# Kernel optimization log

Measured on AMD Instinct MI355X. Metric: run time of the kernel, lower is better.

Reference implementation:

```python
import jax, jax.numpy as jnp
import numpy as np

K, T, CIN = 30000, 35, 7
EPS = 1e-5  # torch BatchNorm default


def _bn(x, gamma, beta):
    # x: [1, K, T, C]; per-channel batch-stat normalization over (0,1,2)
    mean = jnp.mean(x, axis=(0, 1, 2))
    var = jnp.var(x, axis=(0, 1, 2))
    return (x - mean) * jax.lax.rsqrt(var + EPS) * gamma + beta


def _vfe(x, mask, W, b, gamma, beta):
    # x: [1, K, T, Cin] -> [1, K, T, 2*units]
    pw = jnp.einsum('bkti,iu->bktu', x, W) + b
    pw = jax.nn.relu(_bn(pw, gamma, beta))
    agg = jnp.max(pw, axis=2, keepdims=True)            # [1, K, 1, units]
    out = jnp.concatenate([pw, jnp.broadcast_to(agg, pw.shape)], axis=-1)
    return out * mask


def setup_inputs() -> dict:
    key = jax.random.key(0)
    ks = jax.random.split(key, 8)
    inp = {}
    inp['x'] = jax.random.normal(ks[0], (K, T, CIN), jnp.float32)
    inp['coordinate'] = jax.random.randint(ks[1], (K, 4), 0, 1, dtype=jnp.int32)
    inp['batch_size'] = 1
    inp['W1'] = jax.random.normal(ks[2], (7, 16), jnp.float32) * 0.3
    inp['b1'] = jnp.zeros((16,), jnp.float32)
    inp['g1'] = jnp.ones((16,), jnp.float32)
    inp['be1'] = jnp.zeros((16,), jnp.float32)
    inp['W2'] = jax.random.normal(ks[3], (32, 64), jnp.float32) * 0.15
    inp['b2'] = jnp.zeros((64,), jnp.float32)
    inp['g2'] = jnp.ones((64,), jnp.float32)
    inp['be2'] = jnp.zeros((64,), jnp.float32)
    inp['Wd'] = jax.random.normal(ks[4], (128, 128), jnp.float32) * 0.1
    inp['bd'] = jnp.zeros((128,), jnp.float32)
    inp['gd'] = jnp.ones((128,), jnp.float32)
    inp['bed'] = jnp.zeros((128,), jnp.float32)
    return inp


def reference(x, coordinate, batch_size, W1, b1, g1, be1, W2, b2, g2, be2, Wd, bd, gd, bed):
    xb = x[None]                                   # [1, K, T, 7]
    # mask: 1 where the point's feature sum is nonzero
    mask = (jnp.sum(xb, axis=-1) != 0.0).astype(jnp.float32)[..., None]  # [1,K,T,1]
    h = _vfe(xb, mask, W1, b1, g1, be1)            # [1, K, T, 32]
    h = _vfe(h, mask, W2, b2, g2, be2)             # [1, K, T, 128]
    h = jnp.einsum('bktc,cd->bktd', h, Wd) + bd    # [1, K, T, 128]
    h = _bn(h, gd, bed)                            # BatchNorm2d after permute(0,3,1,2)
    h = jnp.where(h >= 0, h, 0.1 * h)              # leaky_relu(0.1)
    h = jnp.max(h, axis=2)                         # max over points -> [1, K, 128]
    out = jnp.transpose(h, (0, 2, 1))              # [1, 128, K] to match NCHW layout
    return (out, coordinate)
```

## Files before the change

### kernel.cpp

```cpp
#include <hip/hip_runtime.h>

#define KVOX 30000
#define TP 35
#define NPTS (KVOX * TP)
#define EPS_BN 1e-5f

typedef __attribute__((ext_vector_type(8))) short short8_t;
typedef __attribute__((ext_vector_type(4))) float f32x4;

#define MFMA_BF16 __builtin_amdgcn_mfma_f32_16x16x32_bf16

#define SLOTG_OFF 0
#define SLOT2_OFF 2560
#define SLOT3_OFF 10752
#define PAR_A1 27136
#define PAR_C1 27152
#define PAR_A2 27168
#define PAR_C2 27232
#define PAR_A3 27296
#define PAR_C3 27424
#define STATS_FLOATS 27136
#define W2T_OFF 27552
#define WDT_OFF 28576
#define M3_OFF 36768
#define SMALL_FLOATS (36768 + KVOX * 64)
#define H1G_OFF SMALL_FLOATS
#define REC_DW 1224
#define FULL_FLOATS (H1G_OFF + (KVOX / 4) * REC_DW)

__device__ __forceinline__ ushort f2bf(float f) {
    uint r;
    asm("v_cvt_pk_bf16_f32 %0, %1, %2" : "=v"(r) : "v"(f), "v"(f));
    return (ushort)r;
}
__device__ __forceinline__ uint f2bf2(float lo, float hi) {
    uint r;
    asm("v_cvt_pk_bf16_f32 %0, %1, %2" : "=v"(r) : "v"(lo), "v"(hi));
    return r;
}
__device__ __forceinline__ float bf2f(ushort h) {
    union { uint u; float f; } v; v.u = ((uint)h) << 16; return v.f;
}
__device__ __forceinline__ f32x4 vmax4(f32x4 a, f32x4 b) {
    f32x4 r;
    r[0] = fmaxf(a[0], b[0]); r[1] = fmaxf(a[1], b[1]);
    r[2] = fmaxf(a[2], b[2]); r[3] = fmaxf(a[3], b[3]);
    return r;
}

__global__ __launch_bounds__(256) void k_prep_stats1(
    const float* __restrict__ x,
    const float* __restrict__ W2, const float* __restrict__ Wd,
    const float* __restrict__ gd,
    ushort* __restrict__ w2t, ushort* __restrict__ wdt,
    float* __restrict__ slotG) {
    if (blockIdx.x < 64) {
        int t = blockIdx.x * 256 + threadIdx.x;
        if (t < 2048) {
            int u = t >> 5, k = t & 31;
            w2t[t] = f2bf(W2[k * 64 + u]);
        }
        int u = t >> 7, k = t & 127;
        float sg = (gd[u] < 0.f) ? -1.f : 1.f;
        wdt[t] = f2bf(Wd[k * 128 + u] * sg);
        return;
    }
    int bid = blockIdx.x - 64;
    int tid = threadIdx.x;
    int gid = bid * 256 + tid;
    float sx[7], G[28];
#pragma unroll
    for (int c = 0; c < 7; ++c) sx[c] = 0.f;
#pragma unroll
    for (int i = 0; i < 28; ++i) G[i] = 0.f;
    for (size_t p4 = (size_t)gid * 4; p4 < NPTS; p4 += (size_t)131072 * 4) {
        const f32x4* xp = (const f32x4*)(x + p4 * 7);
        f32x4 q[7];
#pragma unroll
        for (int c = 0; c < 7; ++c) q[c] = xp[c];
#pragma unroll
        for (int j = 0; j < 4; ++j) {
            float xv[7];
#pragma unroll
            for (int c = 0; c < 7; ++c) {
                int idx = j * 7 + c;
                xv[c] = q[idx >> 2][idx & 3];
                sx[c] += xv[c];
            }
            int idx = 0;
#pragma unroll
            for (int i = 0; i < 7; ++i)
#pragma unroll
                for (int jj = i; jj < 7; ++jj) { G[idx] = fmaf(xv[i], xv[jj], G[idx]); ++idx; }
        }
    }
    int lane = tid & 63;
    int wv = tid >> 6;
    int slot = (bid * 4 + wv) & 63;
#pragma unroll
    for (int k = 0; k < 35; ++k) {
        float v = (k < 28) ? G[k] : sx[k - 28];
#pragma unroll
        for (int m = 32; m > 0; m >>= 1) v += __shfl_xor(v, m, 64);
        if (lane == 0) atomicAdd(&slotG[slot * 40 + k], v);
    }
}

__global__ void k_affine1g(const float* __restrict__ slotG,
                           const float* __restrict__ W1, const float* __restrict__ b1,
                           const float* __restrict__ g1, const float* __restrict__ be1,
                           float* __restrict__ pa, float* __restrict__ pc, float invN) {
    __shared__ float red[35];
    int t = threadIdx.x;
    if (t < 35) {
        float s = 0.f;
#pragma unroll
        for (int sl = 0; sl < 64; ++sl) s += slotG[sl * 40 + t];
        red[t] = s;
    }
    __syncthreads();
    if (t < 16) {
        float wv[7];
#pragma unroll
        for (int c = 0; c < 7; ++c) wv[c] = W1[c * 16 + t];
        float b = b1[t];
        float sw = 0.f;
#pragma unroll
        for (int c = 0; c < 7; ++c) sw = fmaf(red[28 + c], wv[c], sw);
        float gq = 0.f;
        int idx = 0;
#pragma unroll
        for (int i = 0; i < 7; ++i)
#pragma unroll
            for (int j = i; j < 7; ++j) {
                float coef = wv[i] * wv[j];
                if (i != j) coef *= 2.f;
                gq = fmaf(coef, red[idx], gq);
                ++idx;
            }
        float mr = sw * invN;
        float mean = mr + b;
        float ex2 = gq * invN + 2.f * b * mr + b * b;
        float var = ex2 - mean * mean;
        float av = g1[t] * rsqrtf(var + EPS_BN);
        pa[t] = av;
        pc[t] = be1[t] - mean * av;
    }
}

__global__ void k_affine_b(const float* __restrict__ slots,
                           const float* __restrict__ g,
                           const float* __restrict__ be,
                           const float* __restrict__ bias,
                           float* __restrict__ pa, float* __restrict__ pc,
                           int C, float invN) {
    int u = threadIdx.x;
    if (u >= C) return;
    float s = 0.f, q = 0.f;
    for (int sl = 0; sl < 64; ++sl) {
        s += slots[sl * 2 * C + u];
        q += slots[sl * 2 * C + C + u];
    }
    float b = bias[u];
    float mr = s * invN;
    float mean = mr + b;
    float ex2 = q * invN + 2.f * b * mr + b * b;
    float var = ex2 - mean * mean;
    float av = g[u] * rsqrtf(var + EPS_BN);
    pa[u] = av;
    pc[u] = be[u] - mean * av;
}

__global__ void k_affine_b3(const float* __restrict__ slots,
                            const float* __restrict__ g,
                            const float* __restrict__ be,
                            const float* __restrict__ bias,
                            float* __restrict__ pa, float* __restrict__ pc,
                            int C, float invN) {
    int u = threadIdx.x;
    if (u >= C) return;
    float s = 0.f, q = 0.f;
    for (int sl = 0; sl < 64; ++sl) {
        s += slots[sl * 2 * C + u];
        q += slots[sl * 2 * C + C + u];
    }
    float sg = (g[u] < 0.f) ? -1.f : 1.f;
    s *= sg;
    float b = bias[u];
    float mr = s * invN;
    float mean = mr + b;
    float ex2 = q * invN + 2.f * b * mr + b * b;
    float var = ex2 - mean * mean;
    float av = g[u] * rsqrtf(var + EPS_BN);
    pa[u] = av;
    pc[u] = be[u] - mean * av;
}

__device__ __forceinline__ void phaseA4(
    int k0, int tid,
    const float* __restrict__ x,
    const float* __restrict__ W1, const float* __restrict__ b1,
    const float* __restrict__ a1, const float* __restrict__ c1,
    ushort* __restrict__ h1, float* __restrict__ lmask,
    float* __restrict__ aggp , ushort* __restrict__ agg1bf ) {
    int u = tid & 15;
    int g = tid >> 4;
    int v = g & 3;
    int th = g >> 2;
    float pmax = 0.f;
    if (th < 7) {
        float b1u = b1[u];
        float a1u = a1[u], c1u = c1[u];
        float w1c[7];
#pragma unroll
        for (int c = 0; c < 7; ++c) w1c[c] = W1[c * 16 + u];
#pragma unroll
        for (int i = 0; i < 5; ++i) {
            int t = th * 5 + i;
            const float* xp = x + ((size_t)(k0 + v) * TP + t) * 7;
            float xv[7];
            float sum7 = 0.f;
#pragma unroll
            for (int c = 0; c < 7; ++c) { xv[c] = xp[c]; sum7 += xv[c]; }
            float mkv = (sum7 != 0.f) ? 1.f : 0.f;
            int row = 4 * t + v;
            if (u == 0) lmask[row] = mkv;
            float val = b1u;
#pragma unroll
            for (int c = 0; c < 7; ++c) val = fmaf(xv[c], w1c[c], val);
            val = fmaxf(fmaf(a1u, val, c1u), 0.f);
            pmax = fmaxf(pmax, val);
            h1[row * 24 + u] = f2bf(val * mkv);
        }
    } else {
        int row = 140 + v;
        h1[row * 24 + u] = 0;
        if (u == 0) lmask[row] = 0.f;
    }
    int w = tid >> 6;
    int lane = tid & 63;
    if (w < 7) aggp[w * 64 + lane] = pmax;
    __syncthreads();
    if (tid < 64) {
        float m = aggp[tid];
#pragma unroll
        for (int ww = 1; ww < 7; ++ww) m = fmaxf(m, aggp[ww * 64 + tid]);
        agg1bf[tid] = f2bf(m);
    }
    __syncthreads();
}

template <bool DUMP>
__global__ __launch_bounds__(512, 8) void k_stats2(
    const float* __restrict__ x,
    const float* __restrict__ W1, const float* __restrict__ b1,
    const ushort* __restrict__ w2t,
    const float* __restrict__ ws,
    float* __restrict__ slot2, uint* __restrict__ recs) {
    __shared__ __align__(16) ushort h1[144 * 24];
    __shared__ float lmask[144];
    __shared__ float aggp[7 * 64];
    __shared__ __align__(16) ushort agg1bf[64];
    __shared__ __align__(16) uint zeros16[4];
    int tid = threadIdx.x;
    int k0 = blockIdx.x * 4;
    if (tid < 4) zeros16[tid] = 0;
    phaseA4(k0, tid, x, W1, b1, ws + PAR_A1, ws + PAR_C1, h1, lmask, aggp, agg1bf);
    if (DUMP) {
        uint* rec = recs + (size_t)blockIdx.x * REC_DW;
        const uint* h1dw = (const uint*)h1;
        for (int i = tid; i < 1120; i += 512) rec[i] = h1dw[(i >> 3) * 12 + (i & 7)];
        if (tid < 32) rec[1120 + tid] = ((const uint*)agg1bf)[tid];
        if (tid < 70) rec[1152 + tid] = f2bf2(lmask[2 * tid], lmask[2 * tid + 1]);
    }
    int w = tid >> 6, lane = tid & 63, lq = lane >> 4, lr = lane & 15;
    int mh = w >> 2, uq = w & 3;
    int u = uq * 16 + lr;
    short8_t bB = *(const short8_t*)(w2t + u * 32 + (lq & 1) * 8);
    short8_t bP = *(const short8_t*)(w2t + u * 32 + 16 + (lq & 1) * 8);
    const ushort* pap = (lq < 2) ? (agg1bf + (lr & 3) * 16 + (lq & 1) * 8) : (const ushort*)zeros16;
    short8_t pAf = *(const short8_t*)pap;
    f32x4 aP = {0.f, 0.f, 0.f, 0.f};
    aP = MFMA_BF16(pAf, bP, aP, 0, 0, 0);
    f32x4 p1;
    p1[0] = __shfl(aP[0], lr, 64); p1[1] = __shfl(aP[1], lr, 64);
    p1[2] = __shfl(aP[2], lr, 64); p1[3] = __shfl(aP[3], lr, 64);
    f32x4 s1p = {0.f, 0.f, 0.f, 0.f}, s2p = {0.f, 0.f, 0.f, 0.f};
    int mt0 = mh ? 5 : 0, mt1 = mh ? 9 : 5;
    for (int mt = mt0; mt < mt1; ++mt) {
        const ushort* ha = (lq < 2) ? (h1 + (mt * 16 + lr) * 24 + (lq & 1) * 8) : (const ushort*)zeros16;
        short8_t af = *(const short8_t*)ha;
        f32x4 acc = {0.f, 0.f, 0.f, 0.f};
        acc = MFMA_BF16(af, bB, acc, 0, 0, 0);
        f32x4 mk = *(const f32x4*)(lmask + mt * 16 + lq * 4);
        f32x4 am = (acc + p1) * mk;
        s1p += am;
        s2p += am * am;
    }
    float s1 = s1p[0] + s1p[1] + s1p[2] + s1p[3];
    float s2 = s2p[0] + s2p[1] + s2p[2] + s2p[3];
    s1 += __shfl_xor(s1, 16, 64); s1 += __shfl_xor(s1, 32, 64);
    s2 += __shfl_xor(s2, 16, 64); s2 += __shfl_xor(s2, 32, 64);
    if (lq == 0) {
        int slot = blockIdx.x & 63;
        atomicAdd(&slot2[slot * 128 + u], s1);
        atomicAdd(&slot2[slot * 128 + 64 + u], s2);
    }
}

__global__ __launch_bounds__(512, 8) void k_stage3_reuse(
    const uint* __restrict__ recs,
    const float* __restrict__ b2,
    const ushort* __restrict__ w2t, const ushort* __restrict__ wdt,
    const float* __restrict__ bd, const float* __restrict__ gd,
    const float* __restrict__ ws,
    float* __restrict__ slot3, ushort* __restrict__ m3) {
    __shared__ __align__(16) ushort h1[144 * 24];
    __shared__ __align__(16) ushort h2[144 * 72];
    __shared__ float lmask[144];
    __shared__ __align__(16) uint aggfU[4 * 68];
    __shared__ __align__(16) ushort agg1bf[64];
    __shared__ __align__(16) uint zeros16[4];
    int tid = threadIdx.x;
    int k0 = blockIdx.x * 4;
    int w = tid >> 6, lane = tid & 63, lq = lane >> 4, lr = lane & 15;

    {
        const uint* rec = recs + (size_t)blockIdx.x * REC_DW;
        uint* h1dw = (uint*)h1;
        {
            int i = tid;              h1dw[(i >> 3) * 12 + (i & 7)] = rec[i];
            i = tid + 512;            h1dw[(i >> 3) * 12 + (i & 7)] = rec[i];
            i = tid + 1024; if (i < 1120) h1dw[(i >> 3) * 12 + (i & 7)] = rec[i];
        }
        if (tid < 48) h1dw[140 * 12 + tid] = 0u;
        if (tid < 32) ((uint*)agg1bf)[tid] = rec[1120 + tid];
        if (tid < 72) {
            if (tid < 70) {
                uint mw = rec[1152 + tid];
                lmask[2 * tid] = bf2f((ushort)(mw & 0xffffu));
                lmask[2 * tid + 1] = bf2f((ushort)(mw >> 16));
            } else {
                int j = 140 + (tid - 70) * 2;
                lmask[j] = 0.f; lmask[j + 1] = 0.f;
            }
        }
        if (tid < 272) aggfU[tid] = 0u;
        if (tid < 4) zeros16[tid] = 0u;
    }
    __syncthreads();

    {
        int mh = w >> 2, uq = w & 3;
        int u = uq * 16 + lr;
        short8_t bB = *(const short8_t*)(w2t + u * 32 + (lq & 1) * 8);
        short8_t bP = *(const short8_t*)(w2t + u * 32 + 16 + (lq & 1) * 8);
        const ushort* pap = (lq < 2) ? (agg1bf + (lr & 3) * 16 + (lq & 1) * 8) : (const ushort*)zeros16;
        short8_t pAf = *(const short8_t*)pap;
        f32x4 aP = {0.f, 0.f, 0.f, 0.f};
        aP = MFMA_BF16(pAf, bP, aP, 0, 0, 0);
        f32x4 p1;
        p1[0] = __shfl(aP[0], lr, 64); p1[1] = __shfl(aP[1], lr, 64);
        p1[2] = __shfl(aP[2], lr, 64); p1[3] = __shfl(aP[3], lr, 64);
        float a2u = ws[PAR_A2 + u];
        float c2u = fmaf(a2u, b2[u], ws[PAR_C2 + u]);
        f32x4 a2p4 = {a2u, a2u, a2u, a2u};
        f32x4 c2p4 = {c2u, c2u, c2u, c2u};
        f32x4 zero4 = {0.f, 0.f, 0.f, 0.f};
        f32x4 av = {0.f, 0.f, 0.f, 0.f};
        int mt0 = mh ? 5 : 0, mt1 = mh ? 9 : 5;
        for (int mt = mt0; mt < mt1; ++mt) {
            const ushort* ha = (lq < 2) ? (h1 + (mt * 16 + lr) * 24 + (lq & 1) * 8) : (const ushort*)zeros16;
            short8_t af = *(const short8_t*)ha;
            f32x4 acc = {0.f, 0.f, 0.f, 0.f};
            acc = MFMA_BF16(af, bB, acc, 0, 0, 0);
            f32x4 mk = *(const f32x4*)(lmask + mt * 16 + lq * 4);
            int m0 = mt * 16 + lq * 4;
            f32x4 am = (acc + p1) * mk;
            f32x4 val = vmax4(a2p4 * am + c2p4, zero4);
            h2[(m0 + 0) * 72 + u] = f2bf(val[0]);
            h2[(m0 + 1) * 72 + u] = f2bf(val[1]);
            h2[(m0 + 2) * 72 + u] = f2bf(val[2]);
            h2[(m0 + 3) * 72 + u] = f2bf(val[3]);
            if (!(mt == 8 && lq == 3)) av = vmax4(av, val);
        }
#pragma unroll
        for (int r = 0; r < 4; ++r) {
            av[r] = fmaxf(av[r], __shfl_xor(av[r], 16, 64));
            av[r] = fmaxf(av[r], __shfl_xor(av[r], 32, 64));
        }
        if (lq == 0) {
#pragma unroll
            for (int r = 0; r < 4; ++r)
                atomicMax(&aggfU[r * 68 + u], __float_as_uint(av[r]));
        }
    }
    __syncthreads();

    {
        int u = w * 16 + lr;
        short8_t bM0 = *(const short8_t*)(wdt + u * 128 + lq * 8);
        short8_t bM1 = *(const short8_t*)(wdt + u * 128 + 32 + lq * 8);
        short8_t bP0 = *(const short8_t*)(wdt + u * 128 + 64 + lq * 8);
        short8_t bP1 = *(const short8_t*)(wdt + u * 128 + 96 + lq * 8);
        const float* aggf = (const float*)aggfU;
        f32x4 q0 = *(const f32x4*)(aggf + (lr & 3) * 68 + lq * 8);
        f32x4 q1 = *(const f32x4*)(aggf + (lr & 3) * 68 + lq * 8 + 4);
        f32x4 q2 = *(const f32x4*)(aggf + (lr & 3) * 68 + 32 + lq * 8);
        f32x4 q3 = *(const f32x4*)(aggf + (lr & 3) * 68 + 32 + lq * 8 + 4);
        union { uint uu[4]; short8_t s8; } pc0, pc1;
        pc0.uu[0] = f2bf2(q0[0], q0[1]); pc0.uu[1] = f2bf2(q0[2], q0[3]);
        pc0.uu[2] = f2bf2(q1[0], q1[1]); pc0.uu[3] = f2bf2(q1[2], q1[3]);
        pc1.uu[0] = f2bf2(q2[0], q2[1]); pc1.uu[1] = f2bf2(q2[2], q2[3]);
        pc1.uu[2] = f2bf2(q3[0], q3[1]); pc1.uu[3] = f2bf2(q3[2], q3[3]);
        f32x4 aP = {0.f, 0.f, 0.f, 0.f};
        aP = MFMA_BF16(pc0.s8, bP0, aP, 0, 0, 0);
        aP = MFMA_BF16(pc1.s8, bP1, aP, 0, 0, 0);
        f32x4 p2;
        p2[0] = __shfl(aP[0], lr, 64); p2[1] = __shfl(aP[1], lr, 64);
        p2[2] = __shfl(aP[2], lr, 64); p2[3] = __shfl(aP[3], lr, 64);
        f32x4 s1p = {0.f, 0.f, 0.f, 0.f}, s2p = {0.f, 0.f, 0.f, 0.f};
        f32x4 mx = {-1e30f, -1e30f, -1e30f, -1e30f};
#pragma unroll
        for (int mt = 0; mt < 9; ++mt) {
            const ushort* hrow = h2 + (mt * 16 + lr) * 72;
            short8_t a0 = *(const short8_t*)(hrow + lq * 8);
            short8_t a1 = *(const short8_t*)(hrow + 32 + lq * 8);
            f32x4 acc = {0.f, 0.f, 0.f, 0.f};
            acc = MFMA_BF16(a0, bM0, acc, 0, 0, 0);
            acc = MFMA_BF16(a1, bM1, acc, 0, 0, 0);
            f32x4 mk = *(const f32x4*)(lmask + mt * 16 + lq * 4);
            f32x4 am = (acc + p2) * mk;
            s1p += am;
            s2p += am * am;
            if (mt < 8 || lq < 3) mx = vmax4(mx, am);
        }
#pragma unroll
        for (int r = 0; r < 4; ++r) {
            mx[r] = fmaxf(mx[r], __shfl_xor(mx[r], 16, 64));
            mx[r] = fmaxf(mx[r], __shfl_xor(mx[r], 32, 64));
        }
        float s1 = s1p[0] + s1p[1] + s1p[2] + s1p[3];
        float s2 = s2p[0] + s2p[1] + s2p[2] + s2p[3];
        s1 += __shfl_xor(s1, 16, 64); s1 += __shfl_xor(s1, 32, 64);
        s2 += __shfl_xor(s2, 16, 64); s2 += __shfl_xor(s2, 32, 64);
        if (lq == 0) {
            float sg = (gd[u] < 0.f) ? -1.f : 1.f;
            float bdu = bd[u];
#pragma unroll
            for (int r = 0; r < 4; ++r)
                m3[(size_t)(k0 + r) * 128 + u] = f2bf(fmaf(sg, mx[r], bdu));
            int slot = blockIdx.x & 63;
            atomicAdd(&slot3[slot * 256 + u], s1);
            atomicAdd(&slot3[slot * 256 + 128 + u], s2);
        }
    }
}

__device__ __forceinline__ void phaseA_leg(
    int k0, int tid,
    const float* __restrict__ x,
    const float* __restrict__ W1, const float* __restrict__ b1,
    const float* __restrict__ a1, const float* __restrict__ c1,
    ushort* __restrict__ h1, float* __restrict__ lmask, float* __restrict__ aggp) {
    int u = tid & 15;
    int g = tid >> 4;
    int v = g & 1;
    int th = g >> 1;
    float pmax = 0.f;
    if (th < 7) {
        float b1u = b1[u];
        float a1u = a1[u], c1u = c1[u];
        float w1c[7];
#pragma unroll
        for (int c = 0; c < 7; ++c) w1c[c] = W1[c * 16 + u];
#pragma unroll
        for (int i = 0; i < 5; ++i) {
            int t = th * 5 + i;
            const float* xp = x + ((size_t)(k0 + v) * TP + t) * 7;
            float xv[7];
            float sum7 = 0.f;
#pragma unroll
            for (int c = 0; c < 7; ++c) { xv[c] = xp[c]; sum7 += xv[c]; }
            float mkv = (sum7 != 0.f) ? 1.f : 0.f;
            if (u == 0) lmask[v * TP + t] = mkv;
            float val = b1u;
#pragma unroll
            for (int c = 0; c < 7; ++c) val = fmaf(xv[c], w1c[c], val);
            val = fmaxf(fmaf(a1u, val, c1u), 0.f);
            pmax = fmaxf(pmax, val);
            h1[(v * TP + t) * 40 + u] = f2bf(val * mkv);
        }
    } else {
#pragma unroll
        for (int i = 0; i < 5; ++i) {
            int row = 70 + (g & 1) * 5 + i;
            h1[row * 40 + u] = 0;
            if (u == 0) lmask[row] = 0.f;
        }
    }
    pmax = fmaxf(pmax, __shfl_xor(pmax, 32, 64));
    int w = tid >> 6;
    int lane = tid & 63;
    if (lane < 32) aggp[w * 32 + lane] = pmax;
    __syncthreads();
    {
        int uu = tid & 15;
        int r0 = tid >> 4;
        float g0 = fmaxf(fmaxf(aggp[uu], aggp[32 + uu]),
                         fmaxf(aggp[64 + uu], aggp[96 + uu]));
        float g1v = fmaxf(fmaxf(aggp[16 + uu], aggp[48 + uu]),
                          fmaxf(aggp[80 + uu], aggp[112 + uu]));
        ushort a0 = f2bf(g0), a1b = f2bf(g1v);
#pragma unroll
        for (int j = 0; j < 5; ++j) {
            int row = r0 + j * 16;
            float mkv = lmask[row];
            h1[row * 40 + 16 + uu] = (mkv != 0.f) ? ((row < TP) ? a0 : a1b) : (ushort)0;
        }
    }
    __syncthreads();
}

template <bool WSPATH>
__global__ __launch_bounds__(256) void k_stage3_full(
    const float* __restrict__ x,
    const float* __restrict__ W1, const float* __restrict__ b1,
    const float* __restrict__ b2,
    const ushort* __restrict__ w2t, const ushort* __restrict__ wdt,
    const float* __restrict__ bd, const float* __restrict__ gd,
    const float* __restrict__ ws,
    float* __restrict__ slot3,
    ushort* __restrict__ m3, float* __restrict__ outbuf) {
    __shared__ __align__(16) ushort h1[80 * 40];
    __shared__ __align__(16) ushort h2[80 * 136];
    __shared__ float lmask[80];
    __shared__ float aggp[128];
    __shared__ ushort agg2bf[128];
    int tid = threadIdx.x;
    int k0 = blockIdx.x * 2;
    int w = tid >> 6, lane = tid & 63, lq = lane >> 4, lr = lane & 15;
    phaseA_leg(k0, tid, x, W1, b1, ws + PAR_A1, ws + PAR_C1, h1, lmask, aggp);

    int u0 = w * 32;
    short8_t bfr[2][4];
#pragma unroll
    for (int s = 0; s < 2; ++s)
#pragma unroll
        for (int kk = 0; kk < 4; ++kk)
            bfr[s][kk] = *(const short8_t*)(wdt + ((u0 + s * 16 + lr) * 128 + kk * 32 + lq * 8));

    {
        int u = w * 16 + lr;
        short8_t bfrag = *(const short8_t*)(w2t + u * 32 + lq * 8);
        float a2u = ws[PAR_A2 + u];
        float c2p = fmaf(a2u, b2[u], ws[PAR_C2 + u]);
        float aggv0 = 0.f, aggv1 = 0.f;
#pragma unroll
        for (int mt = 0; mt < 5; ++mt) {
            short8_t afrag = *(const short8_t*)(h1 + (mt * 16 + lr) * 40 + lq * 8);
            f32x4 acc = {0.f, 0.f, 0.f, 0.f};
            acc = MFMA_BF16(afrag, bfrag, acc, 0, 0, 0);
#pragma unroll
            for (int r = 0; r < 4; ++r) {
                int m = mt * 16 + lq * 4 + r;
                float val = fmaxf(fmaf(a2u, acc[r], c2p), 0.f);
                float vm = (m < 70) ? val : 0.f;
                if (m < TP) aggv0 = fmaxf(aggv0, vm); else aggv1 = fmaxf(aggv1, vm);
                h2[m * 136 + u] = f2bf(val * lmask[m]);
            }
        }
        aggv0 = fmaxf(aggv0, __shfl_xor(aggv0, 16, 64));
        aggv0 = fmaxf(aggv0, __shfl_xor(aggv0, 32, 64));
        aggv1 = fmaxf(aggv1, __shfl_xor(aggv1, 16, 64));
        aggv1 = fmaxf(aggv1, __shfl_xor(aggv1, 32, 64));
        if (lq == 0) { agg2bf[u] = f2bf(aggv0); agg2bf[64 + u] = f2bf(aggv1); }
    }
    __syncthreads();
    {
        int c = tid & 63;
        int r0 = tid >> 6;
        ushort a0 = agg2bf[c], a1v = agg2bf[64 + c];
#pragma unroll
        for (int j = 0; j < 20; ++j) {
            int row = r0 + j * 4;
            float mkv = lmask[row];
            h2[row * 136 + 64 + c] = (mkv != 0.f) ? ((row < TP) ? a0 : a1v) : (ushort)0;
        }
    }
    __syncthreads();
    {
        float mxa[2][2], s1a[2], s2a[2];
#pragma unroll
        for (int s = 0; s < 2; ++s) {
            s1a[s] = 0.f; s2a[s] = 0.f;
            mxa[s][0] = -1e30f; mxa[s][1] = -1e30f;
        }
#pragma unroll
        for (int mt = 0; mt < 5; ++mt) {
            short8_t af[4];
#pragma unroll
            for (int kk = 0; kk < 4; ++kk)
                af[kk] = *(const short8_t*)(h2 + (mt * 16 + lr) * 136 + kk * 32 + lq * 8);
#pragma unroll
            for (int s = 0; s < 2; ++s) {
                f32x4 acc = {0.f, 0.f, 0.f, 0.f};
#pragma unroll
                for (int kk = 0; kk < 4; ++kk)
                    acc = MFMA_BF16(af[kk], bfr[s][kk], acc, 0, 0, 0);
#pragma unroll
                for (int r = 0; r < 4; ++r) {
                    float a = acc[r];
                    s1a[s] += a;
                    s2a[s] = fmaf(a, a, s2a[s]);
                    int m = mt * 16 + lq * 4 + r;
                    if (mt <= 1) mxa[s][0] = fmaxf(mxa[s][0], a);
                    else if (mt == 3) mxa[s][1] = fmaxf(mxa[s][1], a);
                    else if (mt == 2) { if (m < TP) mxa[s][0] = fmaxf(mxa[s][0], a); else mxa[s][1] = fmaxf(mxa[s][1], a); }
                    else { if (m < 70) mxa[s][1] = fmaxf(mxa[s][1], a); }
                }
            }
        }
#pragma unroll
        for (int s = 0; s < 2; ++s) {
#pragma unroll
            for (int v = 0; v < 2; ++v) {
                mxa[s][v] = fmaxf(mxa[s][v], __shfl_xor(mxa[s][v], 16, 64));
                mxa[s][v] = fmaxf(mxa[s][v], __shfl_xor(mxa[s][v], 32, 64));
            }
            s1a[s] += __shfl_xor(s1a[s], 16, 64); s1a[s] += __shfl_xor(s1a[s], 32, 64);
            s2a[s] += __shfl_xor(s2a[s], 16, 64); s2a[s] += __shfl_xor(s2a[s], 32, 64);
        }
        if (lq == 0) {
            int slot = blockIdx.x & 63;
#pragma unroll
            for (int s = 0; s < 2; ++s) {
                int u = u0 + s * 16 + lr;
                float bdu = bd[u];
                float sg = (gd[u] < 0.f) ? -1.f : 1.f;
#pragma unroll
                for (int v = 0; v < 2; ++v) {
                    float res = fmaf(sg, mxa[s][v], bdu);
                    if (WSPATH) m3[(size_t)(k0 + v) * 128 + u] = f2bf(res);
                    else        outbuf[(size_t)u * KVOX + (k0 + v)] = res;
                }
                atomicAdd(&slot3[slot * 256 + u], s1a[s]);
                atomicAdd(&slot3[slot * 256 + 128 + u], s2a[s]);
            }
        }
    }
}

__global__ __launch_bounds__(256) void k_final_ws(const ushort* __restrict__ m3,
                                                  const float* __restrict__ ws,
                                                  float* __restrict__ out) {
    __shared__ float tile[32][33];
    int tx = threadIdx.x & 31;
    int ty = threadIdx.x >> 5;
    int v0 = blockIdx.x * 32;
    int u0 = blockIdx.y * 32;
    const float* a3 = ws + PAR_A3;
    const float* c3 = ws + PAR_C3;
#pragma unroll
    for (int r = ty; r < 32; r += 8) {
        int v = v0 + r, u = u0 + tx;
        float y = 0.f;
        if (v < KVOX) {
            float a = a3[u], c = c3[u];
            float val = bf2f(m3[(size_t)v * 128 + u]);
            y = a * val + c;
            y = (y >= 0.f) ? y : 0.1f * y;
        }
        tile[r][tx] = y;
    }
    __syncthreads();
#pragma unroll
    for (int r = ty; r < 32; r += 8) {
        int u = u0 + r, v = v0 + tx;
        if (v < KVOX) out[(size_t)u * KVOX + v] = tile[tx][r];
    }
}

__global__ __launch_bounds__(256) void k_final_inplace(const float* __restrict__ ws,
                                                       float* __restrict__ out) {
    int v = blockIdx.x * 256 + threadIdx.x;
    int u = blockIdx.y;
    if (v >= KVOX) return;
    float a = ws[PAR_A3 + u], c = ws[PAR_C3 + u];
    size_t idx = (size_t)u * KVOX + v;
    float y = a * out[idx] + c;
    out[idx] = (y >= 0.f) ? y : 0.1f * y;
}

extern "C" void kernel_launch(void* const* d_in, const int* in_sizes, int n_in,
                              void* d_out, int out_size, void* d_ws, size_t ws_size,
                              hipStream_t stream) {
    const float* x   = (const float*)d_in[0];
    const void*  coord = d_in[1];
    const float* W1  = (const float*)d_in[3];
    const float* b1  = (const float*)d_in[4];
    const float* g1  = (const float*)d_in[5];
    const float* be1 = (const float*)d_in[6];
    const float* W2  = (const float*)d_in[7];
    const float* b2  = (const float*)d_in[8];
    const float* g2  = (const float*)d_in[9];
    const float* be2 = (const float*)d_in[10];
    const float* Wd  = (const float*)d_in[11];
    const float* bd  = (const float*)d_in[12];
    const float* gd  = (const float*)d_in[13];
    const float* bed = (const float*)d_in[14];
    float* ws = (float*)d_ws;
    float* out = (float*)d_out;
    ushort* w2t = (ushort*)(ws + W2T_OFF);
    ushort* wdt = (ushort*)(ws + WDT_OFF);
    ushort* m3  = (ushort*)(ws + M3_OFF);
    uint* recs  = (uint*)(ws + H1G_OFF);

    size_t wsf = ws_size / 4;
    bool full = wsf >= (size_t)FULL_FLOATS;
    bool small = wsf >= (size_t)SMALL_FLOATS;
    const float invN = 1.f / (float)NPTS;

    hipMemsetAsync(d_ws, 0, (size_t)STATS_FLOATS * 4, stream);

    k_prep_stats1<<<64 + 512, 256, 0, stream>>>(x, W2, Wd, gd, w2t, wdt, ws + SLOTG_OFF);
    k_affine1g<<<1, 64, 0, stream>>>(ws + SLOTG_OFF, W1, b1, g1, be1, ws + PAR_A1, ws + PAR_C1, invN);
    if (full)
        k_stats2<true><<<KVOX / 4, 512, 0, stream>>>(x, W1, b1, w2t, ws, ws + SLOT2_OFF, recs);
    else
        k_stats2<false><<<KVOX / 4, 512, 0, stream>>>(x, W1, b1, w2t, ws, ws + SLOT2_OFF, recs);
    k_affine_b<<<1, 64, 0, stream>>>(ws + SLOT2_OFF, g2, be2, b2, ws + PAR_A2, ws + PAR_C2, 64, invN);

    if (full) {
        k_stage3_reuse<<<KVOX / 4, 512, 0, stream>>>(recs, b2, w2t, wdt, bd, gd, ws,
                                                     ws + SLOT3_OFF, m3);
        k_affine_b3<<<1, 128, 0, stream>>>(ws + SLOT3_OFF, gd, bed, bd, ws + PAR_A3, ws + PAR_C3, 128, invN);
        k_final_ws<<<dim3((KVOX + 31) / 32, 4), 256, 0, stream>>>(m3, ws, out);
    } else if (small) {
        k_stage3_full<true><<<KVOX / 2, 256, 0, stream>>>(x, W1, b1, b2, w2t, wdt, bd, gd, ws,
                                                          ws + SLOT3_OFF, m3, out);
        k_affine_b3<<<1, 128, 0, stream>>>(ws + SLOT3_OFF, gd, bed, bd, ws + PAR_A3, ws + PAR_C3, 128, invN);
        k_final_ws<<<dim3((KVOX + 31) / 32, 4), 256, 0, stream>>>(m3, ws, out);
    } else {
        k_stage3_full<false><<<KVOX / 2, 256, 0, stream>>>(x, W1, b1, b2, w2t, wdt, bd, gd, ws,
                                                           ws + SLOT3_OFF, m3, out);
        k_affine_b3<<<1, 128, 0, stream>>>(ws + SLOT3_OFF, gd, bed, bd, ws + PAR_A3, ws + PAR_C3, 128, invN);
        k_final_inplace<<<dim3((KVOX + 255) / 256, 128), 256, 0, stream>>>(ws, out);
    }
    hipMemcpyAsync((char*)d_out + (size_t)128 * KVOX * 4, coord,
                   (size_t)KVOX * 4 * sizeof(int), hipMemcpyDeviceToDevice, stream);
}
```

Measured before the change: 164.4 us.

## Fold BN affine-parameter kernels into consumer kernels and shrink atomic slot count

Removes the separate single-block affine kernels on the main path. Each consumer kernel (stats2, stage3_reuse, final_ws) now reduces the slot partial sums itself and computes its BatchNorm scale/shift into shared memory, which saves three launches and their serialization gaps. Slot count drops from 64 to 16, the stats1 grid is halved, and x loads become unaligned vector reads. In exchange every block redundantly re-reduces the slot sums, and fewer slots means more atomic contention.

Measured after the change: 178.5 us. +8.6%, slower.

```diff
diff --git a/kernel.cpp b/kernel.cpp
--- a/kernel.cpp
+++ b/kernel.cpp
@@ -4,26 +4,29 @@
 #define TP 35
 #define NPTS (KVOX * TP)
 #define EPS_BN 1e-5f
+#define INVN (1.f / (float)NPTS)
+#define NSLOT 16
 
 typedef __attribute__((ext_vector_type(8))) short short8_t;
 typedef __attribute__((ext_vector_type(4))) float f32x4;
+typedef __attribute__((ext_vector_type(4), aligned(4))) float f32x4u;
 
 #define MFMA_BF16 __builtin_amdgcn_mfma_f32_16x16x32_bf16
 
 #define SLOTG_OFF 0
-#define SLOT2_OFF 2560
-#define SLOT3_OFF 10752
-#define PAR_A1 27136
-#define PAR_C1 27152
-#define PAR_A2 27168
-#define PAR_C2 27232
-#define PAR_A3 27296
-#define PAR_C3 27424
-#define STATS_FLOATS 27136
-#define W2T_OFF 27552
-#define WDT_OFF 28576
-#define M3_OFF 36768
-#define SMALL_FLOATS (36768 + KVOX * 64)
+#define SLOT2_OFF 640
+#define SLOT3_OFF 2688
+#define PAR_A1 6784
+#define PAR_C1 6800
+#define PAR_A2 6816
+#define PAR_C2 6880
+#define PAR_A3 6944
+#define PAR_C3 7072
+#define STATS_FLOATS 7200
+#define W2T_OFF 7200
+#define WDT_OFF 8224
+#define M3_OFF 16416
+#define SMALL_FLOATS (16416 + KVOX * 64)
 #define H1G_OFF SMALL_FLOATS
 #define REC_DW 1224
 #define FULL_FLOATS (H1G_OFF + (KVOX / 4) * REC_DW)
@@ -73,8 +76,8 @@
     for (int c = 0; c < 7; ++c) sx[c] = 0.f;
 #pragma unroll
     for (int i = 0; i < 28; ++i) G[i] = 0.f;
-    for (size_t p4 = (size_t)gid * 4; p4 < NPTS; p4 += (size_t)131072 * 4) {
-        const f32x4* xp = (const f32x4*)(x + p4 * 7);
+    for (size_t p4 = (size_t)gid * 4; p4 < NPTS; p4 += (size_t)65536 * 4) {
+        const f32x4u* xp = (const f32x4u*)(x + p4 * 7);
         f32x4 q[7];
 #pragma unroll
         for (int c = 0; c < 7; ++c) q[c] = xp[c];
@@ -96,7 +99,7 @@
     }
     int lane = tid & 63;
     int wv = tid >> 6;
-    int slot = (bid * 4 + wv) & 63;
+    int slot = (bid * 4 + wv) & (NSLOT - 1);
 #pragma unroll
     for (int k = 0; k < 35; ++k) {
         float v = (k < 28) ? G[k] : sx[k - 28];
@@ -104,168 +107,109 @@
         for (int m = 32; m > 0; m >>= 1) v += __shfl_xor(v, m, 64);
         if (lane == 0) atomicAdd(&slotG[slot * 40 + k], v);
     }
-}
-
-__global__ void k_affine1g(const float* __restrict__ slotG,
-                           const float* __restrict__ W1, const float* __restrict__ b1,
-                           const float* __restrict__ g1, const float* __restrict__ be1,
-                           float* __restrict__ pa, float* __restrict__ pc, float invN) {
-    __shared__ float red[35];
-    int t = threadIdx.x;
-    if (t < 35) {
-        float s = 0.f;
-#pragma unroll
-        for (int sl = 0; sl < 64; ++sl) s += slotG[sl * 40 + t];
-        red[t] = s;
-    }
-    __syncthreads();
-    if (t < 16) {
-        float wv[7];
-#pragma unroll
-        for (int c = 0; c < 7; ++c) wv[c] = W1[c * 16 + t];
-        float b = b1[t];
-        float sw = 0.f;
-#pragma unroll
-        for (int c = 0; c < 7; ++c) sw = fmaf(red[28 + c], wv[c], sw);
-        float gq = 0.f;
-        int idx = 0;
-#pragma unroll
-        for (int i = 0; i < 7; ++i)
-#pragma unroll
-            for (int j = i; j < 7; ++j) {
-                float coef = wv[i] * wv[j];
-                if (i != j) coef *= 2.f;
-                gq = fmaf(coef, red[idx], gq);
-                ++idx;
-            }
-        float mr = sw * invN;
-        float mean = mr + b;
-        float ex2 = gq * invN + 2.f * b * mr + b * b;
-        float var = ex2 - mean * mean;
-        float av = g1[t] * rsqrtf(var + EPS_BN);
-        pa[t] = av;
-        pc[t] = be1[t] - mean * av;
-    }
-}
-
-__global__ void k_affine_b(const float* __restrict__ slots,
-                           const float* __restrict__ g,
-                           const float* __restrict__ be,
-                           const float* __restrict__ bias,
-                           float* __restrict__ pa, float* __restrict__ pc,
-                           int C, float invN) {
-    int u = threadIdx.x;
-    if (u >= C) return;
-    float s = 0.f, q = 0.f;
-    for (int sl = 0; sl < 64; ++sl) {
-        s += slots[sl * 2 * C + u];
-        q += slots[sl * 2 * C + C + u];
-    }
-    float b = bias[u];
-    float mr = s * invN;
-    float mean = mr + b;
-    float ex2 = q * invN + 2.f * b * mr + b * b;
-    float var = ex2 - mean * mean;
-    float av = g[u] * rsqrtf(var + EPS_BN);
-    pa[u] = av;
-    pc[u] = be[u] - mean * av;
-}
-
-__global__ void k_affine_b3(const float* __restrict__ slots,
-                            const float* __restrict__ g,
-                            const float* __restrict__ be,
-                            const float* __restrict__ bias,
-                            float* __restrict__ pa, float* __restrict__ pc,
-                            int C, float invN) {
-    int u = threadIdx.x;
-    if (u >= C) return;
-    float s = 0.f, q = 0.f;
-    for (int sl = 0; sl < 64; ++sl) {
-        s += slots[sl * 2 * C + u];
-        q += slots[sl * 2 * C + C + u];
-    }
-    float sg = (g[u] < 0.f) ? -1.f : 1.f;
-    s *= sg;
-    float b = bias[u];
-    float mr = s * invN;
-    float mean = mr + b;
-    float ex2 = q * invN + 2.f * b * mr + b * b;
-    float var = ex2 - mean * mean;
-    float av = g[u] * rsqrtf(var + EPS_BN);
-    pa[u] = av;
-    pc[u] = be[u] - mean * av;
-}
-
-__device__ __forceinline__ void phaseA4(
-    int k0, int tid,
-    const float* __restrict__ x,
-    const float* __restrict__ W1, const float* __restrict__ b1,
-    const float* __restrict__ a1, const float* __restrict__ c1,
-    ushort* __restrict__ h1, float* __restrict__ lmask,
-    float* __restrict__ aggp , ushort* __restrict__ agg1bf ) {
-    int u = tid & 15;
-    int g = tid >> 4;
-    int v = g & 3;
-    int th = g >> 2;
-    float pmax = 0.f;
-    if (th < 7) {
-        float b1u = b1[u];
-        float a1u = a1[u], c1u = c1[u];
-        float w1c[7];
-#pragma unroll
-        for (int c = 0; c < 7; ++c) w1c[c] = W1[c * 16 + u];
-#pragma unroll
-        for (int i = 0; i < 5; ++i) {
-            int t = th * 5 + i;
-            const float* xp = x + ((size_t)(k0 + v) * TP + t) * 7;
-            float xv[7];
-            float sum7 = 0.f;
-#pragma unroll
-            for (int c = 0; c < 7; ++c) { xv[c] = xp[c]; sum7 += xv[c]; }
-            float mkv = (sum7 != 0.f) ? 1.f : 0.f;
-            int row = 4 * t + v;
-            if (u == 0) lmask[row] = mkv;
-            float val = b1u;
-#pragma unroll
-            for (int c = 0; c < 7; ++c) val = fmaf(xv[c], w1c[c], val);
-            val = fmaxf(fmaf(a1u, val, c1u), 0.f);
-            pmax = fmaxf(pmax, val);
-            h1[row * 24 + u] = f2bf(val * mkv);
-        }
-    } else {
-        int row = 140 + v;
-        h1[row * 24 + u] = 0;
-        if (u == 0) lmask[row] = 0.f;
-    }
-    int w = tid >> 6;
-    int lane = tid & 63;
-    if (w < 7) aggp[w * 64 + lane] = pmax;
-    __syncthreads();
-    if (tid < 64) {
-        float m = aggp[tid];
-#pragma unroll
-        for (int ww = 1; ww < 7; ++ww) m = fmaxf(m, aggp[ww * 64 + tid]);
-        agg1bf[tid] = f2bf(m);
-    }
-    __syncthreads();
 }
 
 template <bool DUMP>
 __global__ __launch_bounds__(512, 8) void k_stats2(
     const float* __restrict__ x,
     const float* __restrict__ W1, const float* __restrict__ b1,
+    const float* __restrict__ g1, const float* __restrict__ be1,
     const ushort* __restrict__ w2t,
-    const float* __restrict__ ws,
+    const float* __restrict__ slotG,
     float* __restrict__ slot2, uint* __restrict__ recs) {
     __shared__ __align__(16) ushort h1[144 * 24];
     __shared__ float lmask[144];
     __shared__ float aggp[7 * 64];
     __shared__ __align__(16) ushort agg1bf[64];
     __shared__ __align__(16) uint zeros16[4];
+    __shared__ float red[36], parA1[16], parC1[16];
     int tid = threadIdx.x;
     int k0 = blockIdx.x * 4;
     if (tid < 4) zeros16[tid] = 0;
-    phaseA4(k0, tid, x, W1, b1, ws + PAR_A1, ws + PAR_C1, h1, lmask, aggp, agg1bf);
+    if (tid < 35) {
+        float s = 0.f;
+#pragma unroll
+        for (int sl = 0; sl < NSLOT; ++sl) s += slotG[sl * 40 + tid];
+        red[tid] = s;
+    }
+    __syncthreads();
+    if (tid < 16) {
+        float wv[7];
+#pragma unroll
+        for (int c = 0; c < 7; ++c) wv[c] = W1[c * 16 + tid];
+        float bq = b1[tid];
+        float sw = 0.f;
+#pragma unroll
+        for (int c = 0; c < 7; ++c) sw = fmaf(red[28 + c], wv[c], sw);
+        float gq = 0.f;
+        int idx = 0;
+#pragma unroll
+        for (int ii = 0; ii < 7; ++ii)
+#pragma unroll
+            for (int jj = ii; jj < 7; ++jj) {
+                float coef = wv[ii] * wv[jj];
+                if (ii != jj) coef *= 2.f;
+                gq = fmaf(coef, red[idx], gq);
+                ++idx;
+            }
+        float mr = sw * INVN;
+        float mean = mr + bq;
+        float ex2 = gq * INVN + 2.f * bq * mr + bq * bq;
+        float var = ex2 - mean * mean;
+        float av = g1[tid] * rsqrtf(var + EPS_BN);
+        parA1[tid] = av;
+        parC1[tid] = be1[tid] - mean * av;
+    }
+    __syncthreads();
+    {
+        int u = tid & 15;
+        int g = tid >> 4;
+        int v = g & 3;
+        int th = g >> 2;
+        float pmax = 0.f;
+        if (th < 7) {
+            float b1u = b1[u];
+            float a1u = parA1[u], c1u = parC1[u];
+            float w1c[7];
+#pragma unroll
+            for (int c = 0; c < 7; ++c) w1c[c] = W1[c * 16 + u];
+            const float* pbase = x + (size_t)(k0 + v) * 245 + th * 35;
+#pragma unroll
+            for (int i = 0; i < 5; ++i) {
+                int t = th * 5 + i;
+                f32x4 q0 = *(const f32x4u*)(pbase + i * 7);
+                f32x4 q1 = *(const f32x4u*)(pbase + i * 7 + 3);
+                float xv[7] = {q0[0], q0[1], q0[2], q0[3], q1[1], q1[2], q1[3]};
+                float sum7 = 0.f;
+#pragma unroll
+                for (int c = 0; c < 7; ++c) sum7 += xv[c];
+                float mkv = (sum7 != 0.f) ? 1.f : 0.f;
+                int row = 4 * t + v;
+                if (u == 0) lmask[row] = mkv;
+                float val = b1u;
+#pragma unroll
+                for (int c = 0; c < 7; ++c) val = fmaf(xv[c], w1c[c], val);
+                val = fmaxf(fmaf(a1u, val, c1u), 0.f);
+                pmax = fmaxf(pmax, val);
+                h1[row * 24 + u] = f2bf(val * mkv);
+            }
+        } else {
+            int row = 140 + v;
+            h1[row * 24 + u] = 0;
+            if (u == 0) lmask[row] = 0.f;
+        }
+        int w = tid >> 6;
+        int lane = tid & 63;
+        if (w < 7) aggp[w * 64 + lane] = pmax;
+    }
+    __syncthreads();
+    if (tid < 64) {
+        float m = aggp[tid];
+#pragma unroll
+        for (int ww = 1; ww < 7; ++ww) m = fmaxf(m, aggp[ww * 64 + tid]);
+        agg1bf[tid] = f2bf(m);
+    }
+    __syncthreads();
     if (DUMP) {
         uint* rec = recs + (size_t)blockIdx.x * REC_DW;
         const uint* h1dw = (const uint*)h1;
@@ -302,7 +246,7 @@
     s1 += __shfl_xor(s1, 16, 64); s1 += __shfl_xor(s1, 32, 64);
     s2 += __shfl_xor(s2, 16, 64); s2 += __shfl_xor(s2, 32, 64);
     if (lq == 0) {
-        int slot = blockIdx.x & 63;
+        int slot = blockIdx.x & (NSLOT - 1);
         atomicAdd(&slot2[slot * 128 + u], s1);
         atomicAdd(&slot2[slot * 128 + 64 + u], s2);
     }
@@ -310,10 +254,11 @@
 
 __global__ __launch_bounds__(512, 8) void k_stage3_reuse(
     const uint* __restrict__ recs,
-    const float* __restrict__ b2,
+    const float* __restrict__ b2, const float* __restrict__ g2,
+    const float* __restrict__ be2,
     const ushort* __restrict__ w2t, const ushort* __restrict__ wdt,
     const float* __restrict__ bd, const float* __restrict__ gd,
-    const float* __restrict__ ws,
+    const float* __restrict__ slot2,
     float* __restrict__ slot3, ushort* __restrict__ m3) {
     __shared__ __align__(16) ushort h1[144 * 24];
     __shared__ __align__(16) ushort h2[144 * 72];
@@ -321,6 +266,7 @@
     __shared__ __align__(16) uint aggfU[4 * 68];
     __shared__ __align__(16) ushort agg1bf[64];
     __shared__ __align__(16) uint zeros16[4];
+    __shared__ float parA2L[64], parC2L[64];
     int tid = threadIdx.x;
     int k0 = blockIdx.x * 4;
     int w = tid >> 6, lane = tid & 63, lq = lane >> 4, lr = lane & 15;
@@ -347,6 +293,22 @@
         }
         if (tid < 272) aggfU[tid] = 0u;
         if (tid < 4) zeros16[tid] = 0u;
+        if (tid < 64) {
+            float s = 0.f, q = 0.f;
+#pragma unroll
+            for (int sl = 0; sl < NSLOT; ++sl) {
+                s += slot2[sl * 128 + tid];
+                q += slot2[sl * 128 + 64 + tid];
+            }
+            float bq = b2[tid];
+            float mr = s * INVN;
+            float mean = mr + bq;
+            float ex2 = q * INVN + 2.f * bq * mr + bq * bq;
+            float var = ex2 - mean * mean;
+            float av = g2[tid] * rsqrtf(var + EPS_BN);
+            parA2L[tid] = av;
+            parC2L[tid] = fmaf(av, bq, be2[tid] - mean * av);
+        }
     }
     __syncthreads();
 
@@ -362,8 +324,8 @@
         f32x4 p1;
         p1[0] = __shfl(aP[0], lr, 64); p1[1] = __shfl(aP[1], lr, 64);
         p1[2] = __shfl(aP[2], lr, 64); p1[3] = __shfl(aP[3], lr, 64);
-        float a2u = ws[PAR_A2 + u];
-        float c2u = fmaf(a2u, b2[u], ws[PAR_C2 + u]);
+        float a2u = parA2L[u];
+        float c2u = parC2L[u];
         f32x4 a2p4 = {a2u, a2u, a2u, a2u};
         f32x4 c2p4 = {c2u, c2u, c2u, c2u};
         f32x4 zero4 = {0.f, 0.f, 0.f, 0.f};
@@ -450,11 +412,154 @@
 #pragma unroll
             for (int r = 0; r < 4; ++r)
                 m3[(size_t)(k0 + r) * 128 + u] = f2bf(fmaf(sg, mx[r], bdu));
-            int slot = blockIdx.x & 63;
+            int slot = blockIdx.x & (NSLOT - 1);
             atomicAdd(&slot3[slot * 256 + u], s1);
             atomicAdd(&slot3[slot * 256 + 128 + u], s2);
         }
     }
+}
+
+__global__ __launch_bounds__(256) void k_final_ws(const ushort* __restrict__ m3,
+                                                  const float* __restrict__ slot3,
+                                                  const float* __restrict__ gd,
+                                                  const float* __restrict__ bed,
+                                                  const float* __restrict__ bd,
+                                                  float* __restrict__ out) {
+    __shared__ float tile[32][33];
+    __shared__ float a3L[32], c3L[32];
+    int tid = threadIdx.x;
+    int tx = tid & 31;
+    int ty = tid >> 5;
+    int v0 = blockIdx.x * 32;
+    int u0 = blockIdx.y * 32;
+    if (tid < 32) {
+        int u = u0 + tid;
+        float s = 0.f, q = 0.f;
+#pragma unroll
+        for (int sl = 0; sl < NSLOT; ++sl) {
+            s += slot3[sl * 256 + u];
+            q += slot3[sl * 256 + 128 + u];
+        }
+        float sg = (gd[u] < 0.f) ? -1.f : 1.f;
+        s *= sg;
+        float b = bd[u];
+        float mr = s * INVN;
+        float mean = mr + b;
+        float ex2 = q * INVN + 2.f * b * mr + b * b;
+        float var = ex2 - mean * mean;
+        float av = gd[u] * rsqrtf(var + EPS_BN);
+        a3L[tid] = av;
+        c3L[tid] = bed[u] - mean * av;
+    }
+    __syncthreads();
+#pragma unroll
+    for (int r = ty; r < 32; r += 8) {
+        int v = v0 + r;
+        float y = 0.f;
+        if (v < KVOX) {
+            float a = a3L[tx], c = c3L[tx];
+            float val = bf2f(m3[(size_t)v * 128 + u0 + tx]);
+            y = a * val + c;
+            y = (y >= 0.f) ? y : 0.1f * y;
+        }
+        tile[r][tx] = y;
+    }
+    __syncthreads();
+#pragma unroll
+    for (int r = ty; r < 32; r += 8) {
+        int u = u0 + r, v = v0 + tx;
+        if (v < KVOX) out[(size_t)u * KVOX + v] = tile[tx][r];
+    }
+}
+
+__global__ void k_affine1g(const float* __restrict__ slotG,
+                           const float* __restrict__ W1, const float* __restrict__ b1,
+                           const float* __restrict__ g1, const float* __restrict__ be1,
+                           float* __restrict__ pa, float* __restrict__ pc) {
+    __shared__ float red[35];
+    int t = threadIdx.x;
+    if (t < 35) {
+        float s = 0.f;
+#pragma unroll
+        for (int sl = 0; sl < NSLOT; ++sl) s += slotG[sl * 40 + t];
+        red[t] = s;
+    }
+    __syncthreads();
+    if (t < 16) {
+        float wv[7];
+#pragma unroll
+        for (int c = 0; c < 7; ++c) wv[c] = W1[c * 16 + t];
+        float b = b1[t];
+        float sw = 0.f;
+#pragma unroll
+        for (int c = 0; c < 7; ++c) sw = fmaf(red[28 + c], wv[c], sw);
+        float gq = 0.f;
+        int idx = 0;
+#pragma unroll
+        for (int i = 0; i < 7; ++i)
+#pragma unroll
+            for (int j = i; j < 7; ++j) {
+                float coef = wv[i] * wv[j];
+                if (i != j) coef *= 2.f;
+                gq = fmaf(coef, red[idx], gq);
+                ++idx;
+            }
+        float mr = sw * INVN;
+        float mean = mr + b;
+        float ex2 = gq * INVN + 2.f * b * mr + b * b;
+        float var = ex2 - mean * mean;
+        float av = g1[t] * rsqrtf(var + EPS_BN);
+        pa[t] = av;
+        pc[t] = be1[t] - mean * av;
+    }
+}
+
+__global__ void k_affine_b(const float* __restrict__ slots,
+                           const float* __restrict__ g,
+                           const float* __restrict__ be,
+                           const float* __restrict__ bias,
+                           float* __restrict__ pa, float* __restrict__ pc,
+                           int C) {
+    int u = threadIdx.x;
+    if (u >= C) return;
+    float s = 0.f, q = 0.f;
+    for (int sl = 0; sl < NSLOT; ++sl) {
+        s += slots[sl * 2 * C + u];
+        q += slots[sl * 2 * C + C + u];
+    }
+    float b = bias[u];
+    float mr = s * INVN;
+    float mean = mr + b;
+    float ex2 = q * INVN + 2.f * b * mr + b * b;
+    float var = ex2 - mean * mean;
+    float av = g[u] * rsqrtf(var + EPS_BN);
+    pa[u] = av;
+    pc[u] = be[u] - mean * av;
+}
+
+__global__ void k_affine_b3(const float* __restrict__ slots,
+                            const float* __restrict__ g,
+                            const float* __restrict__ be,
+                            const float* __restrict__ bias,
+                            float* __restrict__ pa, float* __restrict__ pc,
+                            int C) {
+    int u = threadIdx.x;
+    if (u >= C) return;
+    float s = 0.f, q = 0.f;
+    for (int sl = 0; sl < NSLOT; ++sl) {
+        s += slots[sl * 2 * C + u];
+        q += slots[sl * 2 * C + C + u];
+    }
+    float sg = (g[u] < 0.f) ? -1.f : 1.f;
+    s *= sg;
+    float b = bias[u];
+    float mr = s * INVN;
+    float mean = mr + b;
+    float ex2 = q * INVN + 2.f * b * mr + b * b;
+    float var = ex2 - mean * mean;
+    float av = g[u] * rsqrtf(var + EPS_BN);
+    pa[u] = av;
+    pc[u] = be[u] - mean * av;
 }
 
 __device__ __forceinline__ void phaseA_leg(
@@ -522,16 +627,47 @@
     __syncthreads();
 }
 
-template <bool WSPATH>
-__global__ __launch_bounds__(256) void k_stage3_full(
+__global__ __launch_bounds__(256) void k_stats2_fb(
+    const float* __restrict__ x,
+    const float* __restrict__ W1, const float* __restrict__ b1,
+    const ushort* __restrict__ w2t,
+    const float* __restrict__ ws,
+    float* __restrict__ slot2) {
+    __shared__ __align__(16) ushort h1[80 * 40];
+    __shared__ float lmask[80];
+    __shared__ float aggp[128];
+    int tid = threadIdx.x;
+    int k0 = blockIdx.x * 2;
+    phaseA_leg(k0, tid, x, W1, b1, ws + PAR_A1, ws + PAR_C1, h1, lmask, aggp);
+    int w = tid >> 6, lane = tid & 63, lq = lane >> 4, lr = lane & 15;
+    int u = w * 16 + lr;
+    short8_t bfrag = *(const short8_t*)(w2t + u * 32 + lq * 8);
+    float s1v = 0.f, s2v = 0.f;
+#pragma unroll
+    for (int mt = 0; mt < 5; ++mt) {
+        short8_t afrag = *(const short8_t*)(h1 + (mt * 16 + lr) * 40 + lq * 8);
+        f32x4 acc = {0.f, 0.f, 0.f, 0.f};
+        acc = MFMA_BF16(afrag, bfrag, acc, 0, 0, 0);
+#pragma unroll
+        for (int r = 0; r < 4; ++r) { s1v += acc[r]; s2v = fmaf(acc[r], acc[r], s2v); }
+    }
+    s1v += __shfl_xor(s1v, 16, 64); s1v += __shfl_xor(s1v, 32, 64);
+    s2v += __shfl_xor(s2v, 16, 64); s2v += __shfl_xor(s2v, 32, 64);
+    if (lq == 0) {
+        int slot = blockIdx.x & (NSLOT - 1);
+        atomicAdd(&slot2[slot * 128 + u], s1v);
+        atomicAdd(&slot2[slot * 128 + 64 + u], s2v);
+    }
+}
+
+__global__ __launch_bounds__(256) void k_stage3_fb(
     const float* __restrict__ x,
     const float* __restrict__ W1, const float* __restrict__ b1,
     const float* __restrict__ b2,
     const ushort* __restrict__ w2t, const ushort* __restrict__ wdt,
     const float* __restrict__ bd, const float* __restrict__ gd,
     const float* __restrict__ ws,
-    float* __restrict__ slot3,
-    ushort* __restrict__ m3, float* __restrict__ outbuf) {
+    float* __restrict__ slot3, float* __restrict__ outbuf) {
     __shared__ __align__(16) ushort h1[80 * 40];
     __shared__ __align__(16) ushort h2[80 * 136];
     __shared__ float lmask[80];
@@ -541,7 +677,6 @@
     int k0 = blockIdx.x * 2;
     int w = tid >> 6, lane = tid & 63, lq = lane >> 4, lr = lane & 15;
     phaseA_leg(k0, tid, x, W1, b1, ws + PAR_A1, ws + PAR_C1, h1, lmask, aggp);
-
     int u0 = w * 32;
     short8_t bfr[2][4];
 #pragma unroll
@@ -549,7 +684,6 @@
 #pragma unroll
         for (int kk = 0; kk < 4; ++kk)
             bfr[s][kk] = *(const short8_t*)(wdt + ((u0 + s * 16 + lr) * 128 + kk * 32 + lq * 8));
-
     {
         int u = w * 16 + lr;
         short8_t bfrag = *(const short8_t*)(w2t + u * 32 + lq * 8);
@@ -632,52 +766,19 @@
             s2a[s] += __shfl_xor(s2a[s], 16, 64); s2a[s] += __shfl_xor(s2a[s], 32, 64);
         }
         if (lq == 0) {
-            int slot = blockIdx.x & 63;
+            int slot = blockIdx.x & (NSLOT - 1);
 #pragma unroll
             for (int s = 0; s < 2; ++s) {
                 int u = u0 + s * 16 + lr;
                 float bdu = bd[u];
                 float sg = (gd[u] < 0.f) ? -1.f : 1.f;
 #pragma unroll
-                for (int v = 0; v < 2; ++v) {
-                    float res = fmaf(sg, mxa[s][v], bdu);
-                    if (WSPATH) m3[(size_t)(k0 + v) * 128 + u] = f2bf(res);
-                    else        outbuf[(size_t)u * KVOX + (k0 + v)] = res;
-                }
+                for (int v = 0; v < 2; ++v)
+                    outbuf[(size_t)u * KVOX + (k0 + v)] = fmaf(sg, mxa[s][v], bdu);
                 atomicAdd(&slot3[slot * 256 + u], s1a[s]);
                 atomicAdd(&slot3[slot * 256 + 128 + u], s2a[s]);
             }
         }
-    }
-}
-
-__global__ __launch_bounds__(256) void k_final_ws(const ushort* __restrict__ m3,
-                                                  const float* __restrict__ ws,
-                                                  float* __restrict__ out) {
-    __shared__ float tile[32][33];
-    int tx = threadIdx.x & 31;
-    int ty = threadIdx.x >> 5;
-    int v0 = blockIdx.x * 32;
-    int u0 = blockIdx.y * 32;
-    const float* a3 = ws + PAR_A3;
-    const float* c3 = ws + PAR_C3;
-#pragma unroll
-    for (int r = ty; r < 32; r += 8) {
-        int v = v0 + r, u = u0 + tx;
-        float y = 0.f;
-        if (v < KVOX) {
-            float a = a3[u], c = c3[u];
-            float val = bf2f(m3[(size_t)v * 128 + u]);
-            y = a * val + c;
-            y = (y >= 0.f) ? y : 0.1f * y;
-        }
-        tile[r][tx] = y;
-    }
-    __syncthreads();
-#pragma unroll
-    for (int r = ty; r < 32; r += 8) {
-        int u = u0 + r, v = v0 + tx;
-        if (v < KVOX) out[(size_t)u * KVOX + v] = tile[tx][r];
     }
 }
 
@@ -719,33 +820,29 @@
     size_t wsf = ws_size / 4;
     bool full = wsf >= (size_t)FULL_FLOATS;
     bool small = wsf >= (size_t)SMALL_FLOATS;
-    const float invN = 1.f / (float)NPTS;
 
     hipMemsetAsync(d_ws, 0, (size_t)STATS_FLOATS * 4, stream);
-
-    k_prep_stats1<<<64 + 512, 256, 0, stream>>>(x, W2, Wd, gd, w2t, wdt, ws + SLOTG_OFF);
-    k_affine1g<<<1, 64, 0, stream>>>(ws + SLOTG_OFF, W1, b1, g1, be1, ws + PAR_A1, ws + PAR_C1, invN);
-    if (full)
-        k_stats2<true><<<KVOX / 4, 512, 0, stream>>>(x, W1, b1, w2t, ws, ws + SLOT2_OFF, recs);
-    else
-        k_stats2<false><<<KVOX / 4, 512, 0, stream>>>(x, W1, b1, w2t, ws, ws + SLOT2_OFF, recs);
-    k_affine_b<<<1, 64, 0, stream>>>(ws + SLOT2_OFF, g2, be2, b2, ws + PAR_A2, ws + PAR_C2, 64, invN);
+    k_prep_stats1<<<64 + 256, 256, 0, stream>>>(x, W2, Wd, gd, w2t, wdt, ws + SLOTG_OFF);
 
     if (full) {
-        k_stage3_reuse<<<KVOX / 4, 512, 0, stream>>>(recs, b2, w2t, wdt, bd, gd, ws,
-                                                     ws + SLOT3_OFF, m3);
-        k_affine_b3<<<1, 128, 0, stream>>>(ws + SLOT3_OFF, gd, bed, bd, ws + PAR_A3, ws + PAR_C3, 128, invN);
-        k_final_ws<<<dim3((KVOX + 31) / 32, 4), 256, 0, stream>>>(m3, ws, out);
-    } else if (small) {
-        k_stage3_full<true><<<KVOX / 2, 256, 0, stream>>>(x, W1, b1, b2, w2t, wdt, bd, gd, ws,
-                                                          ws + SLOT3_OFF, m3, out);
-        k_affine_b3<<<1, 128, 0, stream>>>(ws + SLOT3_OFF, gd, bed, bd, ws + PAR_A3, ws + PAR_C3, 128, invN);
-        k_final_ws<<<dim3((KVOX + 31) / 32, 4), 256, 0, stream>>>(m3, ws, out);
+        k_stats2<true><<<KVOX / 4, 512, 0, stream>>>(x, W1, b1, g1, be1, w2t,
+                                                     ws + SLOTG_OFF, ws + SLOT2_OFF, recs);
+        k_stage3_reuse<<<KVOX / 4, 512, 0, stream>>>(recs, b2, g2, be2, w2t, wdt, bd, gd,
+                                                     ws + SLOT2_OFF, ws + SLOT3_OFF, m3);
+        k_final_ws<<<dim3((KVOX + 31) / 32, 4), 256, 0, stream>>>(m3, ws + SLOT3_OFF,
+                                                                  gd, bed, bd, out);
     } else {
-        k_stage3_full<false><<<KVOX / 2, 256, 0, stream>>>(x, W1, b1, b2, w2t, wdt, bd, gd, ws,
-                                                           ws + SLOT3_OFF, m3, out);
-        k_affine_b3<<<1, 128, 0, stream>>>(ws + SLOT3_OFF, gd, bed, bd, ws + PAR_A3, ws + PAR_C3, 128, invN);
+        k_affine1g<<<1, 64, 0, stream>>>(ws + SLOTG_OFF, W1, b1, g1, be1,
+                                         ws + PAR_A1, ws + PAR_C1);
+        k_stats2_fb<<<KVOX / 2, 256, 0, stream>>>(x, W1, b1, w2t, ws, ws + SLOT2_OFF);
+        k_affine_b<<<1, 64, 0, stream>>>(ws + SLOT2_OFF, g2, be2, b2,
+                                         ws + PAR_A2, ws + PAR_C2, 64);
+        k_stage3_fb<<<KVOX / 2, 256, 0, stream>>>(x, W1, b1, b2, w2t, wdt, bd, gd, ws,
+                                                  ws + SLOT3_OFF, out);
+        k_affine_b3<<<1, 128, 0, stream>>>(ws + SLOT3_OFF, gd, bed, bd,
+                                           ws + PAR_A3, ws + PAR_C3, 128);
         k_final_inplace<<<dim3((KVOX + 255) / 256, 128), 256, 0, stream>>>(ws, out);
+        (void)small;
     }
     hipMemcpyAsync((char*)d_out + (size_t)128 * KVOX * 4, coord,
                    (size_t)KVOX * 4 * sizeof(int), hipMemcpyDeviceToDevice, stream);
```
